# Optimization experiments

Hardware: AMD Instinct MI355X
Metric: run time of the kernel (lower is better)

## Reference

```python
import jax, jax.numpy as jnp
import numpy as np
import math

EPS = 1e-06
H = W = 28


def _cell_id(cell):
    Hc, Wc = H // cell, W // cell
    yy = np.arange(H)[:, None]
    xx = np.arange(W)[None, :]
    cy = np.clip(yy // cell, 0, Hc - 1)
    cx = np.clip(xx // cell, 0, Wc - 1)
    return Hc, Wc, jnp.asarray((cy * Wc + cx).astype(np.int32))


def _sobel(x):
    # x: [B,1,28,28], zero-padded 3x3 Sobel, scaled by 1/4
    p = jnp.pad(x, ((0, 0), (0, 0), (1, 1), (1, 1)))
    gx = (p[..., :-2, :-2] + 2.0 * p[..., 1:-1, :-2] + p[..., 2:, :-2]
          - p[..., :-2, 2:] - 2.0 * p[..., 1:-1, 2:] - p[..., 2:, 2:]) * 0.25
    gy = (p[..., :-2, :-2] + 2.0 * p[..., :-2, 1:-1] + p[..., :-2, 2:]
          - p[..., 2:, :-2] - 2.0 * p[..., 2:, 1:-1] - p[..., 2:, 2:]) * 0.25
    return gx, gy


def _hog_generic(gx, gy, bins, cell, eps):
    B = gx.shape[0]
    mag = jnp.sqrt(gx * gx + gy * gy + eps)
    ang = jnp.arctan2(gy, gx) * (180.0 / math.pi)
    ang = (ang + 180.0) % 180.0
    Hc, Wc, cell_id = _cell_id(cell)
    bin_w = 180.0 / bins
    b0 = jnp.clip(jnp.floor(ang / bin_w), 0, bins - 1).astype(jnp.int32)
    frac = (ang - b0.astype(ang.dtype) * bin_w) / bin_w
    b1 = (b0 + 1) % bins
    base = (jnp.arange(B, dtype=jnp.int32) * (Hc * Wc)).reshape(B, 1, 1, 1)
    dest = base + cell_id[None, None, :, :]  # [B,1,H,W]
    m = mag.reshape(-1)
    f = frac.reshape(-1)
    d = dest.reshape(-1)
    idx0 = d * bins + b0.reshape(-1)
    idx1 = d * bins + b1.reshape(-1)
    nseg = B * Hc * Wc * bins
    # single fused scatter-add for both soft-assigned bins
    hist_1d = jax.ops.segment_sum(
        jnp.concatenate([m * (1.0 - f), m * f]),
        jnp.concatenate([idx0, idx1]),
        num_segments=nseg,
    )
    hist = hist_1d.reshape(B, Hc, Wc, bins)
    blk = jnp.stack(
        [hist[:, :-1, :-1, :], hist[:, :-1, 1:, :],
         hist[:, 1:, :-1, :], hist[:, 1:, 1:, :]],
        axis=-2,
    ).reshape(B, Hc - 1, Wc - 1, 4 * bins)
    norm = jnp.sqrt(jnp.sum(blk * blk, axis=-1, keepdims=True) + 1e-06)
    blk = jnp.minimum(blk / norm, 0.2)  # L2-hys clip
    norm2 = jnp.sqrt(jnp.sum(blk * blk, axis=-1, keepdims=True) + 1e-06)
    blk = blk / norm2
    return blk.reshape(B, -1)


def setup_inputs() -> dict:
    key = jax.random.key(0)
    k1, k2 = jax.random.split(key)
    B = 16384
    x = jax.random.uniform(k1, (B, 1, 28, 28), dtype=jnp.float32)
    feat_dim = 784 + 1152 + 2304 + 4056
    feat_mean = jnp.zeros((feat_dim,), dtype=jnp.float32)
    feat_std = jnp.ones((feat_dim,), dtype=jnp.float32)
    return {"x": x, "feat_mean": feat_mean, "feat_std": feat_std}


def reference(x, feat_mean, feat_std):
    x = x.astype(jnp.float32)
    gx, gy = _sobel(x)
    h4 = _hog_generic(gx, gy, bins=8, cell=4, eps=EPS)   # [B,1152]
    h3 = _hog_generic(gx, gy, bins=9, cell=3, eps=EPS)   # [B,2304]
    h2 = _hog_generic(gx, gy, bins=6, cell=2, eps=EPS)   # [B,4056]
    flat = x.reshape(x.shape[0], -1)                      # [B,784]
    feat = jnp.concatenate([flat, h4, h3, h2], axis=1)    # [B,8296]
    return (feat - feat_mean) / feat_std
```

## Files before the change

kernel.cpp:

```cpp
#include <hip/hip_runtime.h>
#include <math.h>


constexpr int NPIX = 784;
constexpr int FEAT = 8296;
constexpr int PB4 = 9, PB3 = 10, PB2 = 7;
constexpr int O4P = 0, O3P = 441, O2P = 1251;
constexpr int HIST_TOT = 2623;
constexpr int NTASK = 269;
constexpr int NHOG = FEAT - NPIX;
constexpr int NCELL = 49 + 81 + 196;

__device__ __forceinline__ int feat_map(int i) {
    int task, h;
    if (i < 1936) {
        int k = i - 784;
        int t = k >> 5, r = k & 31;
        int q = r >> 3, j = r & 7;
        int by = t / 6, bx = t - by * 6;
        h = O4P + ((by + (q >> 1)) * 7 + bx + (q & 1)) * PB4 + j;
        task = t;
    } else if (i < 4240) {
        int k = i - 1936;
        int t = k / 36, r = k - t * 36;
        int q = r / 9,  j = r - q * 9;
        int by = t >> 3, bx = t & 7;
        h = O3P + ((by + (q >> 1)) * 9 + bx + (q & 1)) * PB3 + j;
        task = 36 + t;
    } else {
        int k = i - 4240;
        int t = k / 24, r = k - t * 24;
        int q = r / 6,  j = r - q * 6;
        int by = t / 13, bx = t - by * 13;
        h = O2P + ((by + (q >> 1)) * 14 + bx + (q & 1)) * PB2 + j;
        task = 100 + t;
    }
    return (task << 12) | h;
}

__global__ __launch_bounds__(256)
void setup_kernel(const float* __restrict__ fmean,
                  const float* __restrict__ fstd,
                  float2* __restrict__ msr, int* __restrict__ map) {
    int i = blockIdx.x * 256 + threadIdx.x;
    if (i < FEAT) {
        msr[i] = make_float2(fmean[i], 1.0f / fstd[i]);
        if (i >= NPIX) map[i - NPIX] = feat_map(i);
    }
}

__device__ __forceinline__ float orient_deg(float gy, float gx) {
    float ax = fabsf(gx), ay = fabsf(gy);
    float mn = fminf(ax, ay), mx = fmaxf(ax, ay);
    float r = __fdividef(mn, mx + 1e-37f);
    float a = r * r;
    float th = ((((0.0208351f * a - 0.0851330f) * a + 0.1801410f) * a
                 - 0.3302995f) * a + 0.9998660f) * r;
    th *= 57.29577951308232f;
    if (ay > ax) th = 90.0f - th;
    bool neg = ((__float_as_uint(gx) ^ __float_as_uint(gy)) >> 31) != 0;
    float o = neg ? 180.0f - th : th;
    return (o >= 180.0f) ? 0.0f : o;
}

__device__ __forceinline__ float ldimg(const float* img, int y, int x) {
    return (y >= 0 && y < 28 && x >= 0 && x < 28) ? img[y * 28 + x] : 0.0f;
}

template <bool USE_TABLE>
__global__ __launch_bounds__(256)
void hog_kernel(const float* __restrict__ x,
                const float* __restrict__ fmean,
                const float* __restrict__ fstd,
                const float2* __restrict__ msr,
                const int* __restrict__ map,
                float* __restrict__ out) {
    __shared__ __align__(16) float img[NPIX];
    __shared__ __align__(16) float2 ma[NPIX];
    __shared__ float hist[HIST_TOT];
    __shared__ float2 nrm[NTASK];

    const int b = blockIdx.x;
    const int tid = threadIdx.x;
    const float* xb = x + (size_t)b * NPIX;

    for (int i = tid; i < NPIX / 4; i += 256)
        reinterpret_cast<float4*>(img)[i] =
            reinterpret_cast<const float4*>(xb)[i];
    __syncthreads();

    for (int p = tid; p < NPIX; p += 256) {
        int y = p / 28, xx = p - (p / 28) * 28;
        float a00 = ldimg(img, y - 1, xx - 1);
        float a01 = ldimg(img, y - 1, xx);
        float a02 = ldimg(img, y - 1, xx + 1);
        float a10 = ldimg(img, y,     xx - 1);
        float a12 = ldimg(img, y,     xx + 1);
        float a20 = ldimg(img, y + 1, xx - 1);
        float a21 = ldimg(img, y + 1, xx);
        float a22 = ldimg(img, y + 1, xx + 1);
        float gxv = (a00 + 2.0f * a10 + a20 - a02 - 2.0f * a12 - a22) * 0.25f;
        float gyv = (a00 + 2.0f * a01 + a02 - a20 - 2.0f * a21 - a22) * 0.25f;
        float mag = sqrtf(gxv * gxv + gyv * gyv + 1e-6f);
        ma[p] = make_float2(mag, orient_deg(gyv, gxv));
    }
    __syncthreads();

    for (int t = tid; t < NCELL; t += 256) {
        int base, y0, x0, ny, nx, bins;
        float invbw;
        if (t < 49) {
            int cy = t / 7, cx = t - cy * 7;
            y0 = cy * 4; x0 = cx * 4; ny = 4; nx = 4;
            bins = 8; invbw = 8.0f / 180.0f;
            base = O4P + t * PB4;
        } else if (t < 130) {
            int k = t - 49;
            int cy = k / 9, cx = k - cy * 9;
            y0 = cy * 3; x0 = cx * 3;
            ny = (cy == 8) ? 4 : 3; nx = (cx == 8) ? 4 : 3;
            bins = 9; invbw = 9.0f / 180.0f;
            base = O3P + k * PB3;
        } else {
            int k = t - 130;
            int cy = k / 14, cx = k - cy * 14;
            y0 = cy * 2; x0 = cx * 2; ny = 2; nx = 2;
            bins = 6; invbw = 6.0f / 180.0f;
            base = O2P + k * PB2;
        }
        for (int j = 0; j < bins; ++j) hist[base + j] = 0.0f;
        for (int iy = 0; iy < ny; ++iy) {
            int row = (y0 + iy) * 28 + x0;
            for (int ix = 0; ix < nx; ++ix) {
                float2 m = ma[row + ix];
                float tb = m.y * invbw;
                int b0 = (int)tb;
                if (b0 > bins - 1) b0 = bins - 1;
                float frac = tb - (float)b0;
                float w1 = m.x * frac;
                float w0 = m.x - w1;
                int b1 = b0 + 1; if (b1 == bins) b1 = 0;
                hist[base + b0] += w0;
                hist[base + b1] += w1;
            }
        }
    }
    __syncthreads();

    for (int t = tid; t < NTASK; t += 256) {
        int bins, Wc, pb, hoff, by, bx;
        if (t < 36)       { bins = 8; pb = PB4; Wc = 7;  hoff = O4P;
                            by = t / 6; bx = t - by * 6; }
        else if (t < 100) { int k = t - 36; bins = 9; pb = PB3; Wc = 9; hoff = O3P;
                            by = k >> 3; bx = k & 7; }
        else              { int k = t - 100; bins = 6; pb = PB2; Wc = 14; hoff = O2P;
                            by = k / 13; bx = k - by * 13; }
        int c00 = hoff + (by * Wc + bx) * pb;
        int cb[4] = {c00, c00 + pb, c00 + Wc * pb, c00 + (Wc + 1) * pb};

        float s = 0.0f;
        #pragma unroll
        for (int q = 0; q < 4; ++q)
            for (int j = 0; j < bins; ++j) {
                float v = hist[cb[q] + j];
                s += v * v;
            }
        float ninv = 1.0f / sqrtf(s + 1e-6f);

        float s2 = 0.0f;
        #pragma unroll
        for (int q = 0; q < 4; ++q)
            for (int j = 0; j < bins; ++j) {
                float c = fminf(hist[cb[q] + j] * ninv, 0.2f);
                s2 += c * c;
            }
        nrm[t] = make_float2(ninv, 1.0f / sqrtf(s2 + 1e-6f));
    }
    __syncthreads();

    float4* outp = reinterpret_cast<float4*>(out + (size_t)b * FEAT);

    for (int i4 = tid; i4 < NPIX / 4; i4 += 256) {
        float4 v = reinterpret_cast<const float4*>(img)[i4];
        float4 r;
        if (USE_TABLE) {
            const float4* msr4 = reinterpret_cast<const float4*>(msr);
            float4 p0 = msr4[i4 * 2], p1 = msr4[i4 * 2 + 1];
            r.x = (v.x - p0.x) * p0.y;  r.y = (v.y - p0.z) * p0.w;
            r.z = (v.z - p1.x) * p1.y;  r.w = (v.w - p1.z) * p1.w;
        } else {
            int i = i4 * 4;
            r.x = (v.x - fmean[i])     / fstd[i];
            r.y = (v.y - fmean[i + 1]) / fstd[i + 1];
            r.z = (v.z - fmean[i + 2]) / fstd[i + 2];
            r.w = (v.w - fmean[i + 3]) / fstd[i + 3];
        }
        outp[i4] = r;
    }

    for (int t4 = tid; t4 < NHOG / 4; t4 += 256) {
        int i4 = NPIX / 4 + t4;
        int mp[4];
        if (USE_TABLE) {
            int4 m4 = reinterpret_cast<const int4*>(map)[t4];
            mp[0] = m4.x; mp[1] = m4.y; mp[2] = m4.z; mp[3] = m4.w;
        } else {
            #pragma unroll
            for (int e = 0; e < 4; ++e) mp[e] = feat_map(i4 * 4 + e);
        }
        float vv[4];
        #pragma unroll
        for (int e = 0; e < 4; ++e) {
            int task = mp[e] >> 12, h = mp[e] & 4095;
            float2 n = nrm[task];
            vv[e] = fminf(hist[h] * n.x, 0.2f) * n.y;
        }
        float4 r;
        if (USE_TABLE) {
            const float4* msr4 = reinterpret_cast<const float4*>(msr);
            float4 p0 = msr4[i4 * 2], p1 = msr4[i4 * 2 + 1];
            r.x = (vv[0] - p0.x) * p0.y;  r.y = (vv[1] - p0.z) * p0.w;
            r.z = (vv[2] - p1.x) * p1.y;  r.w = (vv[3] - p1.z) * p1.w;
        } else {
            int i = i4 * 4;
            r.x = (vv[0] - fmean[i])     / fstd[i];
            r.y = (vv[1] - fmean[i + 1]) / fstd[i + 1];
            r.z = (vv[2] - fmean[i + 2]) / fstd[i + 2];
            r.w = (vv[3] - fmean[i + 3]) / fstd[i + 3];
        }
        outp[i4] = r;
    }
}

extern "C" void kernel_launch(void* const* d_in, const int* in_sizes, int n_in,
                              void* d_out, int out_size, void* d_ws, size_t ws_size,
                              hipStream_t stream) {
    const float* x     = (const float*)d_in[0];
    const float* fmean = (const float*)d_in[1];
    const float* fstd  = (const float*)d_in[2];
    float* out = (float*)d_out;
    int B = in_sizes[0] / NPIX;

    const size_t msr_bytes = (size_t)FEAT * sizeof(float2);
    const size_t map_bytes = (size_t)NHOG * sizeof(int);
    if (ws_size >= msr_bytes + map_bytes) {
        float2* msr = (float2*)d_ws;
        int* map = (int*)((char*)d_ws + msr_bytes);
        hipLaunchKernelGGL(setup_kernel, dim3((FEAT + 255) / 256), dim3(256),
                           0, stream, fmean, fstd, msr, map);
        hipLaunchKernelGGL(hog_kernel<true>, dim3(B), dim3(256), 0, stream,
                           x, fmean, fstd, msr, map, out);
    } else {
        hipLaunchKernelGGL(hog_kernel<false>, dim3(B), dim3(256), 0, stream,
                           x, fmean, fstd, nullptr, nullptr, out);
    }
}
```

Measured before the change: 205.5 us.

## Drop shared image staging, pad histograms with wrap bin, template block normalisation

Removes the shared-memory image buffer and its sync, so the Sobel stencil and the raw-pixel output read the input straight from global memory and cache. Histograms get a uniform 10-float stride with an extra overflow bin that is folded back into bin 0 after accumulation, which removes the clamp and wrap branches from the binning loop. Block normalisation is templated on bin count, loading values into registers once instead of reading shared memory twice. Launch bounds now request 6 blocks per CU, trading register headroom and larger hist shared usage for occupancy; repeated global stencil loads may cost more than the removed shared staging.

Measured after the change: 272.8 us. 1.33x slower.

```diff
diff --git a/kernel.cpp b/kernel.cpp
--- a/kernel.cpp
+++ b/kernel.cpp
@@ -4,9 +4,11 @@
 
 constexpr int NPIX = 784;
 constexpr int FEAT = 8296;
-constexpr int PB4 = 9, PB3 = 10, PB2 = 7;
-constexpr int O4P = 0, O3P = 441, O2P = 1251;
-constexpr int HIST_TOT = 2623;
+constexpr int PB  = 10;
+constexpr int O4P = 0;
+constexpr int O3P = 490;
+constexpr int O2P = 1300;
+constexpr int HIST_TOT = 1300 + 1960;
 constexpr int NTASK = 269;
 constexpr int NHOG = FEAT - NPIX;
 constexpr int NCELL = 49 + 81 + 196;
@@ -18,21 +20,21 @@
         int t = k >> 5, r = k & 31;
         int q = r >> 3, j = r & 7;
         int by = t / 6, bx = t - by * 6;
-        h = O4P + ((by + (q >> 1)) * 7 + bx + (q & 1)) * PB4 + j;
+        h = O4P + ((by + (q >> 1)) * 7 + bx + (q & 1)) * PB + j;
         task = t;
     } else if (i < 4240) {
         int k = i - 1936;
         int t = k / 36, r = k - t * 36;
         int q = r / 9,  j = r - q * 9;
         int by = t >> 3, bx = t & 7;
-        h = O3P + ((by + (q >> 1)) * 9 + bx + (q & 1)) * PB3 + j;
+        h = O3P + ((by + (q >> 1)) * 9 + bx + (q & 1)) * PB + j;
         task = 36 + t;
     } else {
         int k = i - 4240;
         int t = k / 24, r = k - t * 24;
         int q = r / 6,  j = r - q * 6;
         int by = t / 13, bx = t - by * 13;
-        h = O2P + ((by + (q >> 1)) * 14 + bx + (q & 1)) * PB2 + j;
+        h = O2P + ((by + (q >> 1)) * 14 + bx + (q & 1)) * PB + j;
         task = 100 + t;
     }
     return (task << 12) | h;
@@ -63,19 +65,43 @@
     return (o >= 180.0f) ? 0.0f : o;
 }
 
-__device__ __forceinline__ float ldimg(const float* img, int y, int x) {
-    return (y >= 0 && y < 28 && x >= 0 && x < 28) ? img[y * 28 + x] : 0.0f;
+__device__ __forceinline__ float ldx(const float* xb, int y, int x) {
+    return (y >= 0 && y < 28 && x >= 0 && x < 28) ? xb[y * 28 + x] : 0.0f;
+}
+
+template <int BINS>
+__device__ __forceinline__ float2 norm_task(const float* hist, int hoff,
+                                            int Wc, int by, int bx) {
+    int c00 = hoff + (by * Wc + bx) * PB;
+    float v[4 * BINS];
+    #pragma unroll
+    for (int q = 0; q < 4; ++q) {
+        int base = c00 + ((q >> 1) * Wc + (q & 1)) * PB;
+        #pragma unroll
+        for (int j = 0; j < BINS; ++j)
+            v[q * BINS + j] = hist[base + j];
+    }
+    float s = 1e-6f;
+    #pragma unroll
+    for (int k = 0; k < 4 * BINS; ++k) s += v[k] * v[k];
+    float ninv = 1.0f / sqrtf(s);
+    float s2 = 1e-6f;
+    #pragma unroll
+    for (int k = 0; k < 4 * BINS; ++k) {
+        float c = fminf(v[k] * ninv, 0.2f);
+        s2 += c * c;
+    }
+    return make_float2(ninv, 1.0f / sqrtf(s2));
 }
 
 template <bool USE_TABLE>
-__global__ __launch_bounds__(256)
+__global__ __launch_bounds__(256, 6)
 void hog_kernel(const float* __restrict__ x,
                 const float* __restrict__ fmean,
                 const float* __restrict__ fstd,
                 const float2* __restrict__ msr,
                 const int* __restrict__ map,
                 float* __restrict__ out) {
-    __shared__ __align__(16) float img[NPIX];
     __shared__ __align__(16) float2 ma[NPIX];
     __shared__ float hist[HIST_TOT];
     __shared__ float2 nrm[NTASK];
@@ -84,21 +110,16 @@
     const int tid = threadIdx.x;
     const float* xb = x + (size_t)b * NPIX;
 
-    for (int i = tid; i < NPIX / 4; i += 256)
-        reinterpret_cast<float4*>(img)[i] =
-            reinterpret_cast<const float4*>(xb)[i];
-    __syncthreads();
-
     for (int p = tid; p < NPIX; p += 256) {
         int y = p / 28, xx = p - (p / 28) * 28;
-        float a00 = ldimg(img, y - 1, xx - 1);
-        float a01 = ldimg(img, y - 1, xx);
-        float a02 = ldimg(img, y - 1, xx + 1);
-        float a10 = ldimg(img, y,     xx - 1);
-        float a12 = ldimg(img, y,     xx + 1);
-        float a20 = ldimg(img, y + 1, xx - 1);
-        float a21 = ldimg(img, y + 1, xx);
-        float a22 = ldimg(img, y + 1, xx + 1);
+        float a00 = ldx(xb, y - 1, xx - 1);
+        float a01 = ldx(xb, y - 1, xx);
+        float a02 = ldx(xb, y - 1, xx + 1);
+        float a10 = ldx(xb, y,     xx - 1);
+        float a12 = ldx(xb, y,     xx + 1);
+        float a20 = ldx(xb, y + 1, xx - 1);
+        float a21 = ldx(xb, y + 1, xx);
+        float a22 = ldx(xb, y + 1, xx + 1);
         float gxv = (a00 + 2.0f * a10 + a20 - a02 - 2.0f * a12 - a22) * 0.25f;
         float gyv = (a00 + 2.0f * a01 + a02 - a20 - 2.0f * a21 - a22) * 0.25f;
         float mag = sqrtf(gxv * gxv + gyv * gyv + 1e-6f);
@@ -113,75 +134,63 @@
             int cy = t / 7, cx = t - cy * 7;
             y0 = cy * 4; x0 = cx * 4; ny = 4; nx = 4;
             bins = 8; invbw = 8.0f / 180.0f;
-            base = O4P + t * PB4;
+            base = O4P + t * PB;
         } else if (t < 130) {
             int k = t - 49;
             int cy = k / 9, cx = k - cy * 9;
             y0 = cy * 3; x0 = cx * 3;
             ny = (cy == 8) ? 4 : 3; nx = (cx == 8) ? 4 : 3;
             bins = 9; invbw = 9.0f / 180.0f;
-            base = O3P + k * PB3;
+            base = O3P + k * PB;
         } else {
             int k = t - 130;
             int cy = k / 14, cx = k - cy * 14;
             y0 = cy * 2; x0 = cx * 2; ny = 2; nx = 2;
             bins = 6; invbw = 6.0f / 180.0f;
-            base = O2P + k * PB2;
-        }
-        for (int j = 0; j < bins; ++j) hist[base + j] = 0.0f;
+            base = O2P + k * PB;
+        }
+        for (int j = 0; j <= bins; ++j) hist[base + j] = 0.0f;
         for (int iy = 0; iy < ny; ++iy) {
             int row = (y0 + iy) * 28 + x0;
             for (int ix = 0; ix < nx; ++ix) {
                 float2 m = ma[row + ix];
                 float tb = m.y * invbw;
                 int b0 = (int)tb;
-                if (b0 > bins - 1) b0 = bins - 1;
                 float frac = tb - (float)b0;
                 float w1 = m.x * frac;
                 float w0 = m.x - w1;
-                int b1 = b0 + 1; if (b1 == bins) b1 = 0;
-                hist[base + b0] += w0;
-                hist[base + b1] += w1;
+                int a = base + b0;
+                float h0 = hist[a];
+                float h1 = hist[a + 1];
+                hist[a]     = h0 + w0;
+                hist[a + 1] = h1 + w1;
             }
         }
+        hist[base] += hist[base + bins];
     }
     __syncthreads();
 
     for (int t = tid; t < NTASK; t += 256) {
-        int bins, Wc, pb, hoff, by, bx;
-        if (t < 36)       { bins = 8; pb = PB4; Wc = 7;  hoff = O4P;
-                            by = t / 6; bx = t - by * 6; }
-        else if (t < 100) { int k = t - 36; bins = 9; pb = PB3; Wc = 9; hoff = O3P;
-                            by = k >> 3; bx = k & 7; }
-        else              { int k = t - 100; bins = 6; pb = PB2; Wc = 14; hoff = O2P;
-                            by = k / 13; bx = k - by * 13; }
-        int c00 = hoff + (by * Wc + bx) * pb;
-        int cb[4] = {c00, c00 + pb, c00 + Wc * pb, c00 + (Wc + 1) * pb};
-
-        float s = 0.0f;
-        #pragma unroll
-        for (int q = 0; q < 4; ++q)
-            for (int j = 0; j < bins; ++j) {
-                float v = hist[cb[q] + j];
-                s += v * v;
-            }
-        float ninv = 1.0f / sqrtf(s + 1e-6f);
-
-        float s2 = 0.0f;
-        #pragma unroll
-        for (int q = 0; q < 4; ++q)
-            for (int j = 0; j < bins; ++j) {
-                float c = fminf(hist[cb[q] + j] * ninv, 0.2f);
-                s2 += c * c;
-            }
-        nrm[t] = make_float2(ninv, 1.0f / sqrtf(s2 + 1e-6f));
+        float2 r;
+        if (t < 36) {
+            int by = t / 6, bx = t - (t / 6) * 6;
+            r = norm_task<8>(hist, O4P, 7, by, bx);
+        } else if (t < 100) {
+            int k = t - 36;
+            r = norm_task<9>(hist, O3P, 9, k >> 3, k & 7);
+        } else {
+            int k = t - 100;
+            int by = k / 13, bx = k - by * 13;
+            r = norm_task<6>(hist, O2P, 14, by, bx);
+        }
+        nrm[t] = r;
     }
     __syncthreads();
 
     float4* outp = reinterpret_cast<float4*>(out + (size_t)b * FEAT);
 
     for (int i4 = tid; i4 < NPIX / 4; i4 += 256) {
-        float4 v = reinterpret_cast<const float4*>(img)[i4];
+        float4 v = reinterpret_cast<const float4*>(xb)[i4];
         float4 r;
         if (USE_TABLE) {
             const float4* msr4 = reinterpret_cast<const float4*>(msr);
```
